# Performance work log

Hardware: AMD Instinct MI355X
Metric: run time of the kernel (lower is better)

Reference implementation:

```python
import math
import jax, jax.numpy as jnp
import numpy as np

B, S, HIDDEN = 1, 8192, 2048
NUM_HEADS = 16
HEAD_DIM = HIDDEN // NUM_HEADS
NUM_FW = 4
FW_DIM = HIDDEN // NUM_FW
D_H = FW_DIM  # inter_multi = 1.0
WINDOW = 256
CHUNK = 2048
ROPE_THETA = 500000.0
BASE_LR_INV = float(np.log(np.expm1(0.001)))  # inv_softplus(1e-3)


def rms_norm(x, w, eps=1e-6):
    return x * jax.lax.rsqrt(jnp.mean(x * x, axis=-1, keepdims=True) + eps) * w


def apply_rope(q, k, theta):
    D = q.shape[-1]
    inv = 1.0 / (theta ** (jnp.arange(0, D, 2, dtype=jnp.float32) / D))
    t = jnp.arange(q.shape[1], dtype=jnp.float32)
    f = t[:, None] * inv[None, :]  # [S, D/2]
    cos = jnp.cos(f)[None, :, None, :]
    sin = jnp.sin(f)[None, :, None, :]
    def ap(x):
        x1, x2 = jnp.split(x, 2, axis=-1)
        return jnp.concatenate([x1 * cos - x2 * sin, x2 * cos + x1 * sin], axis=-1)
    return ap(q), ap(k)


def sliding_window_attn(q, k, v, window):
    # q,k,v: [B,S,H,D]; causal window of `window` tokens incl. self (flash (window-1, 0))
    B_, S_, H_, D_ = q.shape
    W = window
    nc = S_ // W
    def blk(x):
        return x.transpose(0, 2, 1, 3).reshape(B_, H_, nc, W, D_)
    qb, kb, vb = blk(q), blk(k), blk(v)
    pad = jnp.zeros((B_, H_, 1, W, D_), q.dtype)
    k2 = jnp.concatenate([jnp.concatenate([pad, kb[:, :, :-1]], 2), kb], 3)  # [B,H,nc,2W,D]
    v2 = jnp.concatenate([jnp.concatenate([pad, vb[:, :, :-1]], 2), vb], 3)
    r = jnp.arange(W)[:, None]
    j = jnp.arange(2 * W)[None, :]
    base = (j >= r + 1) & (j <= W + r)  # causal + within-window
    keypos = (jnp.arange(nc)[:, None, None] - 1) * W + j[None]
    mask = base[None] & (keypos >= 0)  # [nc,W,2W]
    scores = jnp.einsum('bhnqd,bhnkd->bhnqk', qb, k2) * (1.0 / math.sqrt(D_))
    scores = jnp.where(mask[None, None], scores, -jnp.inf)
    p = jax.nn.softmax(scores, axis=-1)
    o = jnp.einsum('bhnqk,bhnkd->bhnqd', p, v2)
    return o.reshape(B_, H_, S_, D_).transpose(0, 2, 1, 3)


def ttt_swiglu(fq, fk, fv, l0, l1, l2, w0, w1, w2, chunk):
    # fq/fk/fv: [BN,S,d]; l*: [BN,S,1]; w0,w2: [BN,dh,d]; w1: [BN,d,dh]
    BN, S_, d = fq.shape
    nc = S_ // chunk
    def ch(x):
        return x.reshape(BN, nc, chunk, x.shape[-1]).transpose(1, 0, 2, 3)
    xs = (ch(fq), ch(fk), ch(fv), ch(l0), ch(l1), ch(l2))
    def step(carry, x):
        w0c, w1c, w2c = carry
        qi, ki, vi, lr0, lr1, lr2 = x
        # apply current fast weights to chunk queries (SwiGLU MLP)
        o = jnp.einsum('bch,boh->bco',
                       jax.nn.silu(jnp.einsum('bcd,bhd->bch', qi, w0c)) * jnp.einsum('bcd,bhd->bch', qi, w2c),
                       w1c)
        # manual gradient of dot-product TTT loss L = -sum(v * f(k))
        g = jnp.einsum('bcd,bhd->bch', ki, w0c)
        hm = jnp.einsum('bcd,bhd->bch', ki, w2c)
        sg = jax.nn.sigmoid(g)
        silu_g = g * sg
        hid = silu_g * hm
        dhid = jnp.einsum('bco,boh->bch', vi, w1c)
        dhm = dhid * silu_g
        dg = dhid * hm
        dgp = dg * (sg * (1.0 + g * (1.0 - sg)))  # silu backprop
        w0n = w0c + jnp.einsum('bch,bcd->bhd', dgp * lr0, ki)
        w2n = w2c + jnp.einsum('bch,bcd->bhd', dhm * lr2, ki)
        w1n = w1c + jnp.einsum('bco,bch->boh', vi * lr1, hid)
        return (w0n, w1n, w2n), o
    _, outs = jax.lax.scan(step, (w0, w1, w2), xs)
    return outs.transpose(1, 0, 2, 3).reshape(BN, S_, d)


def setup_inputs():
    key = jax.random.key(0)
    ks = jax.random.split(key, 8)
    h = HIDDEN
    return {
        'hidden_states': jax.random.normal(ks[0], (B, S, h), jnp.float32),
        'qkv_w': jax.random.normal(ks[1], (3 * h, h), jnp.float32) * 0.02,
        'q_norm_w': jnp.ones((h,), jnp.float32),
        'k_norm_w': jnp.ones((h,), jnp.float32),
        'qk_scale': jnp.ones((h, 2), jnp.float32),
        'qk_offset': jnp.zeros((h, 2), jnp.float32),
        'lr_w': jax.random.normal(ks[2], (3 * NUM_FW, h), jnp.float32) * 0.02,
        'lr_b': jnp.zeros((3 * NUM_FW,), jnp.float32),
        'w0': jax.random.normal(ks[3], (NUM_FW, D_H, FW_DIM), jnp.float32) / math.sqrt(FW_DIM),
        'w1': jax.random.normal(ks[4], (NUM_FW, FW_DIM, D_H), jnp.float32) / math.sqrt(D_H),
        'w2': jax.random.normal(ks[5], (NUM_FW, D_H, FW_DIM), jnp.float32) / math.sqrt(FW_DIM),
        'ttt_norm_w': jnp.ones((FW_DIM,), jnp.float32),
        'o_proj_w': jax.random.normal(ks[6], (h, h), jnp.float32) * 0.02,
    }


def reference(hidden_states, qkv_w, q_norm_w, k_norm_w, qk_scale, qk_offset,
              lr_w, lr_b, w0, w1, w2, ttt_norm_w, o_proj_w):
    qkv = hidden_states @ qkv_w.T
    q, k, v = jnp.split(qkv, 3, axis=-1)
    q = rms_norm(q, q_norm_w)
    k = rms_norm(k, k_norm_w)
    # rescale q/k for the fast-weight path
    fq = q * qk_scale[:, 0] + qk_offset[:, 0]
    fk = k * qk_scale[:, 1] + qk_offset[:, 1]
    fv = v
    # windowed RoPE attention path
    qh = q.reshape(B, S, NUM_HEADS, HEAD_DIM)
    kh = k.reshape(B, S, NUM_HEADS, HEAD_DIM)
    vh = v.reshape(B, S, NUM_HEADS, HEAD_DIM)
    qh, kh = apply_rope(qh, kh, ROPE_THETA)
    attn_o = sliding_window_attn(qh, kh, vh, WINDOW).reshape(B, S, HIDDEN)
    # fast-weight (TTT) path: silu + per-head l2-norm on q/k
    fq = jax.nn.silu(fq).reshape(B, S, NUM_FW, FW_DIM)
    fk = jax.nn.silu(fk).reshape(B, S, NUM_FW, FW_DIM)
    fv = jax.nn.silu(fv).reshape(B, S, NUM_FW, FW_DIM)
    fq = fq / jnp.maximum(jnp.linalg.norm(fq, axis=-1, keepdims=True), 1e-12)
    fk = fk / jnp.maximum(jnp.linalg.norm(fk, axis=-1, keepdims=True), 1e-12)
    def flat(x):
        return x.transpose(0, 2, 1, 3).reshape(B * NUM_FW, S, FW_DIM)
    # per-token learning rates (mamba parameterization)
    lr = jax.nn.softplus(hidden_states @ lr_w.T + lr_b + BASE_LR_INV)  # [B,S,3*NH]
    l0, l1, l2 = jnp.split(lr, 3, axis=-1)
    def flat_lr(x):
        return x.transpose(0, 2, 1).reshape(B * NUM_FW, S, 1)
    def bcast(w):
        return jnp.broadcast_to(w[None], (B,) + w.shape).reshape(B * NUM_FW, w.shape[1], w.shape[2])
    o_fast = ttt_swiglu(flat(fq), flat(fk), flat(fv),
                        flat_lr(l0), flat_lr(l1), flat_lr(l2),
                        bcast(w0), bcast(w1), bcast(w2), CHUNK)
    o_fast = rms_norm(o_fast.reshape(B, NUM_FW, S, FW_DIM), ttt_norm_w)
    o_fast = o_fast.transpose(0, 2, 1, 3).reshape(B, S, HIDDEN)
    return (attn_o + o_fast) @ o_proj_w.T
```

## Files before the change

### kernel.cpp

```cpp
#include <hip/hip_runtime.h>
#include <hip/hip_bf16.h>

typedef __hip_bfloat16 bf16;
typedef __bf16 bft;
typedef bft bf16x8 __attribute__((ext_vector_type(8)));
typedef bft bf16x4 __attribute__((ext_vector_type(4)));
typedef float f32x4 __attribute__((ext_vector_type(4)));

#define S_LEN 8192
#define HID   2048
#define QKV3  6144
#define NH    16
#define HD    128
#define NFW   4
#define FD    512
#define CHUNK_LEN 2048
#define NCHUNK 4
#define BASE_LR_INV (-6.9072552f)
#define QKP 136
#define VSP 72
#define PSP 76

__device__ __forceinline__ float bf2f(bf16 x){ return __bfloat162float(x); }
__device__ __forceinline__ bf16  f2bf(float x){ return __float2bfloat16(x); }
__device__ __forceinline__ float sigm(float x){ return 1.f/(1.f+__expf(-x)); }
__device__ __forceinline__ float siluf(float x){ return x/(1.f+__expf(-x)); }
__device__ __forceinline__ float wave_sum(float v){
  #pragma unroll
  for(int off=32; off; off>>=1) v += __shfl_xor(v, off, 64);
  return v;
}

template<int N>
__device__ __forceinline__ void waitcnt_vm(){
  static_assert(N==0||N==2||N==4||N==8, "unsupported vmcnt");
  if constexpr (N==0)      asm volatile("s_waitcnt vmcnt(0)" ::: "memory");
  else if constexpr (N==2) asm volatile("s_waitcnt vmcnt(2)" ::: "memory");
  else if constexpr (N==4) asm volatile("s_waitcnt vmcnt(4)" ::: "memory");
  else                     asm volatile("s_waitcnt vmcnt(8)" ::: "memory");
}

__device__ __forceinline__ void bar(){
  __builtin_amdgcn_s_barrier();
  asm volatile("" ::: "memory");
}

template<int ROWS>
__device__ __forceinline__ void stage(const bft* __restrict__ src, long ld,
                                      bft* dst, int tid)
{
  const int lane = tid & 63, wv = tid >> 6;
  #pragma unroll
  for (int i = 0; i < ROWS/64; ++i) {
    const int r0 = wv*16 + i*64;
    const int row = r0 + (lane >> 2);
    const int g = (lane & 3) ^ ((row >> 1) & 3);
    const bft* gp = src + (size_t)row*ld + g*8;
    bft* lp = dst + (size_t)r0*32;
    __builtin_amdgcn_global_load_lds(
        (const __attribute__((address_space(1))) void*)gp,
        (__attribute__((address_space(3))) void*)lp, 16, 0, 0);
  }
}

template<int BM,int BN,int EPI>
__global__ __launch_bounds__(256) void mgemm_k(
    const bft* __restrict__ A, const bft* __restrict__ B, void* __restrict__ Cv,
    bft* __restrict__ Cd, bft* __restrict__ Ct, int K,
    long lda, long ldb, long ldc, long sA, long sB, long sC)
{
  constexpr int AM = BM/32, AN = BN/32;
  constexpr int LPT = BM/64 + BN/64;
  constexpr int NPH = (AM >= 4) ? 2 : 1;
  constexpr int MH  = AM / NPH;
  __shared__ __align__(16) bft As[4][BM*32];
  __shared__ __align__(16) bft Bs[4][BN*32];
  const int tid = threadIdx.x;
  const int z = blockIdx.z;
  A += (size_t)z * sA;
  B += (size_t)z * sB;
  const size_t m0 = (size_t)blockIdx.y * BM, n0 = (size_t)blockIdx.x * BN;
  const int wv = tid >> 6, lane = tid & 63;
  const int wm = (wv & 1) * (BM/2), wn = (wv >> 1) * (BN/2);
  const int fr = lane & 15;
  const int fsw = ((lane >> 4) ^ ((fr >> 1) & 3)) * 8;

  f32x4 acc[AM][AN];
  #pragma unroll
  for (int i=0;i<AM;i++)
    #pragma unroll
    for (int j=0;j<AN;j++) acc[i][j] = (f32x4){0.f,0.f,0.f,0.f};

  const bft* Ab = A + m0*lda;
  const bft* Bb = B + n0*ldb;
  const int NS = K >> 5;

  stage<BM>(Ab,      lda, As[0], tid);
  stage<BN>(Bb,      ldb, Bs[0], tid);
  stage<BM>(Ab + 32, lda, As[1], tid);
  stage<BN>(Bb + 32, ldb, Bs[1], tid);
  waitcnt_vm<LPT>();
  bar();

  for (int s = 0; s < NS; ++s) {
    const bft* Ap = As[s & 3];
    const bft* Bp = Bs[s & 3];
    const int kt = (s + 2) * 32;
    const bool st = (s + 2 < NS);

    bf16x8 bvv[AN], afv[MH];
    #pragma unroll
    for (int ni=0; ni<AN; ni++)
      bvv[ni] = *(const bf16x8*)(Bp + (size_t)(wn + ni*16 + fr)*32 + fsw);
    #pragma unroll
    for (int i=0; i<MH; i++)
      afv[i] = *(const bf16x8*)(Ap + (size_t)(wm + i*16 + fr)*32 + fsw);
    if (st) stage<BM>(Ab + kt, lda, As[(s+2)&3], tid);
    if constexpr (NPH == 1) {
      if (st) { stage<BN>(Bb + kt, ldb, Bs[(s+2)&3], tid); waitcnt_vm<LPT>(); }
      else waitcnt_vm<0>();
    }
    bar();
    __builtin_amdgcn_s_setprio(1);
    #pragma unroll
    for (int i=0; i<MH; i++)
      #pragma unroll
      for (int ni=0; ni<AN; ni++)
        acc[i][ni] = __builtin_amdgcn_mfma_f32_16x16x32_bf16(afv[i], bvv[ni], acc[i][ni], 0, 0, 0);
    __builtin_amdgcn_s_setprio(0);

    if constexpr (NPH == 2) {
      bar();
      #pragma unroll
      for (int i=0; i<MH; i++)
        afv[i] = *(const bf16x8*)(Ap + (size_t)(wm + (MH+i)*16 + fr)*32 + fsw);
      if (st) { stage<BN>(Bb + kt, ldb, Bs[(s+2)&3], tid); waitcnt_vm<LPT>(); }
      else waitcnt_vm<0>();
      bar();
      __builtin_amdgcn_s_setprio(1);
      #pragma unroll
      for (int i=0; i<MH; i++)
        #pragma unroll
        for (int ni=0; ni<AN; ni++)
          acc[MH+i][ni] = __builtin_amdgcn_mfma_f32_16x16x32_bf16(afv[i], bvv[ni], acc[MH+i][ni], 0, 0, 0);
      __builtin_amdgcn_s_setprio(0);
      bar();
    }
  }

  const int er = (lane >> 4) * 4;
  const int ec = lane & 15;
  #pragma unroll
  for (int mi=0; mi<AM; mi++){
    #pragma unroll
    for (int ni=0; ni<AN; ni++){
      #pragma unroll
      for (int r=0; r<4; r++){
        size_t row = m0 + wm + mi*16 + er + r;
        size_t col = n0 + wn + ni*16 + ec;
        size_t idx = (size_t)z*sC + row*ldc + col;
        float v = acc[mi][ni][r];
        if constexpr (EPI == 0){
          ((bft*)Cv)[idx] = (bft)v;
        } else if constexpr (EPI == 1){
          ((float*)Cv)[idx] = v;
        } else {
          float nv = ((float*)Cv)[idx] + v;
          ((float*)Cv)[idx] = nv;
          Cd[idx] = (bft)nv;
          if (Ct) Ct[(size_t)z*FD*FD + col*FD + row] = (bft)nv;
        }
      }
    }
  }
}

template<int BM,int BN,int EPI>
static inline void mgemm(hipStream_t st, const bft* A, const bft* B, void* C,
    bft* Cd, bft* Ct, int M, int N, int K, long lda, long ldb, long ldc,
    int batch, long sA, long sB, long sC)
{
  dim3 g(N/BN, M/BM, batch);
  mgemm_k<BM,BN,EPI><<<g, 256, 0, st>>>(A, B, C, Cd, Ct, K, lda, ldb, ldc, sA, sB, sC);
}

__device__ __forceinline__ void stage8(const bft* __restrict__ src, long ld,
                                       bft* dst, int tid)
{
  const int lane = tid & 63, wv = tid >> 6;
  #pragma unroll
  for (int i = 0; i < 2; ++i) {
    const int r0 = wv*16 + i*128;
    const int row = r0 + (lane >> 2);
    const int g = (lane & 3) ^ ((row >> 1) & 3);
    const bft* gp = src + (size_t)row*ld + g*8;
    bft* lp = dst + (size_t)r0*32;
    __builtin_amdgcn_global_load_lds(
        (const __attribute__((address_space(1))) void*)gp,
        (__attribute__((address_space(3))) void*)lp, 16, 0, 0);
  }
}

#define M8_ROW(mi, a) { \
    acc[mi][0]=__builtin_amdgcn_mfma_f32_16x16x32_bf16(a,bv[0],acc[mi][0],0,0,0); \
    acc[mi][1]=__builtin_amdgcn_mfma_f32_16x16x32_bf16(a,bv[1],acc[mi][1],0,0,0); \
    acc[mi][2]=__builtin_amdgcn_mfma_f32_16x16x32_bf16(a,bv[2],acc[mi][2],0,0,0); \
    acc[mi][3]=__builtin_amdgcn_mfma_f32_16x16x32_bf16(a,bv[3],acc[mi][3],0,0,0); }

template<int EPI>
__global__ __launch_bounds__(512, 2) void mgemm8_k(
    const bft* __restrict__ A, const bft* __restrict__ B, void* __restrict__ Cv,
    int K, long lda, long ldb, long ldc)
{
  __shared__ __align__(16) bft As[4][256*32];
  __shared__ __align__(16) bft Bs[4][256*32];
  const int tid = threadIdx.x;

  const int gx = (int)gridDim.x;
  const int nwg = (int)(gridDim.x * gridDim.y);
  int lin = (int)(blockIdx.y * gridDim.x + blockIdx.x);
  if ((nwg & 7) == 0) lin = (lin & 7) * (nwg >> 3) + (lin >> 3);
  const size_t m0 = (size_t)(lin / gx) * 256;
  const size_t n0 = (size_t)(lin % gx) * 256;

  const int wv = tid >> 6, lane = tid & 63;
  const int wm = (wv & 1) * 128, wn = (wv >> 1) * 64;
  const int fr = lane & 15;
  const int fsw = ((lane >> 4) ^ ((fr >> 1) & 3)) * 8;

  f32x4 acc[8][4];
  #pragma unroll
  for (int i=0;i<8;i++)
    #pragma unroll
    for (int j=0;j<4;j++) acc[i][j] = (f32x4){0.f,0.f,0.f,0.f};

  const bft* Ab = A + m0*lda;
  const bft* Bb = B + n0*ldb;
  const int NS = K >> 5;

  stage8(Ab,      lda, As[0], tid);
  stage8(Bb,      ldb, Bs[0], tid);
  stage8(Ab + 32, lda, As[1], tid);
  stage8(Bb + 32, ldb, Bs[1], tid);
  waitcnt_vm<4>();
  bar();

  for (int s = 0; s < NS; ++s) {
    const bft* Ap = As[s & 3];
    const bft* Bp = Bs[s & 3];
    const int kt = (s + 2) * 32;
    const bool st = (s + 2 < NS);
    bf16x8 bv[4], a0, a1, a2, a3;

    bv[0] = *(const bf16x8*)(Bp + (size_t)(wn +  0 + fr)*32 + fsw);
    bv[1] = *(const bf16x8*)(Bp + (size_t)(wn + 16 + fr)*32 + fsw);
    bv[2] = *(const bf16x8*)(Bp + (size_t)(wn + 32 + fr)*32 + fsw);
    bv[3] = *(const bf16x8*)(Bp + (size_t)(wn + 48 + fr)*32 + fsw);
    a0 = *(const bf16x8*)(Ap + (size_t)(wm +  0 + fr)*32 + fsw);
    a1 = *(const bf16x8*)(Ap + (size_t)(wm + 16 + fr)*32 + fsw);
    a2 = *(const bf16x8*)(Ap + (size_t)(wm + 32 + fr)*32 + fsw);
    a3 = *(const bf16x8*)(Ap + (size_t)(wm + 48 + fr)*32 + fsw);
    if (st) stage8(Ab + kt, lda, As[(s+2)&3], tid);
    bar();
    __builtin_amdgcn_s_setprio(1);
    M8_ROW(0, a0); M8_ROW(1, a1); M8_ROW(2, a2); M8_ROW(3, a3);
    __builtin_amdgcn_s_setprio(0);
    bar();

    a0 = *(const bf16x8*)(Ap + (size_t)(wm +  64 + fr)*32 + fsw);
    a1 = *(const bf16x8*)(Ap + (size_t)(wm +  80 + fr)*32 + fsw);
    a2 = *(const bf16x8*)(Ap + (size_t)(wm +  96 + fr)*32 + fsw);
    a3 = *(const bf16x8*)(Ap + (size_t)(wm + 112 + fr)*32 + fsw);
    if (st) { stage8(Bb + kt, ldb, Bs[(s+2)&3], tid); waitcnt_vm<4>(); }
    else waitcnt_vm<0>();
    bar();
    __builtin_amdgcn_s_setprio(1);
    M8_ROW(4, a0); M8_ROW(5, a1); M8_ROW(6, a2); M8_ROW(7, a3);
    __builtin_amdgcn_s_setprio(0);
    bar();
  }

  const int er = (lane >> 4) * 4;
  const int ec = lane & 15;
  #pragma unroll
  for (int mi=0; mi<8; mi++){
    #pragma unroll
    for (int ni=0; ni<4; ni++){
      #pragma unroll
      for (int r=0; r<4; r++){
        size_t row = m0 + wm + mi*16 + er + r;
        size_t col = n0 + wn + ni*16 + ec;
        size_t idx = row*ldc + col;
        float v = acc[mi][ni][r];
        if constexpr (EPI == 0) ((bft*)Cv)[idx] = (bft)v;
        else                    ((float*)Cv)[idx] = v;
      }
    }
  }
}

template<int EPI>
static inline void mgemm8(hipStream_t st, const bft* A, const bft* B, void* C,
                          int M, int N, int K, long lda, long ldb, long ldc)
{
  dim3 g(N/256, M/256, 1);
  mgemm8_k<EPI><<<g, 512, 0, st>>>(A, B, C, K, lda, ldb, ldc);
}

__global__ __launch_bounds__(256) void cvt_k(const float* __restrict__ s,
    bft* __restrict__ d)
{
  size_t i = ((size_t)blockIdx.x*256 + threadIdx.x) * 8;
  const float4 v0 = *(const float4*)(s + i);
  const float4 v1 = *(const float4*)(s + i + 4);
  bf16x8 b;
  b[0]=(bft)v0.x; b[1]=(bft)v0.y; b[2]=(bft)v0.z; b[3]=(bft)v0.w;
  b[4]=(bft)v1.x; b[5]=(bft)v1.y; b[6]=(bft)v1.z; b[7]=(bft)v1.w;
  *(bf16x8*)(d + i) = b;
}

__global__ __launch_bounds__(256) void tr_k(const bft* __restrict__ in,
    bft* __restrict__ out, long ldin, long sIn, long sOut)
{
  __shared__ __align__(16) bft t[64][72];
  const int c0 = blockIdx.x*64, r0 = blockIdx.y*64;
  in  += (size_t)blockIdx.z * sIn;
  out += (size_t)blockIdx.z * sOut;
  const int tid = threadIdx.x;
  #pragma unroll
  for (int i=0;i<2;i++){
    int e = tid + i*256;
    int r = e >> 3, c8 = (e & 7) * 8;
    *(bf16x8*)&t[r][c8] = *(const bf16x8*)(in + (size_t)(r0+r)*ldin + c0 + c8);
  }
  __syncthreads();
  #pragma unroll
  for (int i=0;i<2;i++){
    int e = tid + i*256;
    int c = e >> 3, r8 = (e & 7) * 8;
    bf16x8 v;
    #pragma unroll
    for (int j=0;j<8;j++) v[j] = t[r8+j][c];
    *(bf16x8*)(out + (size_t)(c0+c)*CHUNK_LEN + r0 + r8) = v;
  }
}

__global__ __launch_bounds__(256) void tcw1_k(const float* __restrict__ w1,
    bft* __restrict__ w1tb)
{
  size_t idx = (size_t)blockIdx.x*256 + threadIdx.x;
  int z = (int)(idx >> 18);
  int h = (int)((idx >> 9) & 511);
  int o = (int)(idx & 511);
  w1tb[idx] = (bft)w1[(size_t)z*FD*FD + (size_t)o*FD + h];
}

__global__ __launch_bounds__(256) void vt_k(const bf16* __restrict__ qkv,
    bft* __restrict__ vT)
{
  __shared__ __align__(16) bft t[64*QKP];
  const int s0 = blockIdx.x * 64;
  const int h  = blockIdx.y;
  const int tid = threadIdx.x;
  #pragma unroll
  for (int i=0;i<4;i++){
    int e = tid + i*256;
    int rr = e >> 4, doff = (e & 15) * 8;
    *(bf16x8*)(t + rr*QKP + doff) =
        *(const bf16x8*)((const bft*)qkv + (size_t)(s0+rr)*QKV3 + 2*HID + h*HD + doff);
  }
  __syncthreads();
  #pragma unroll
  for (int it=0; it<4; it++){
    int d = (tid >> 3) + it*32;
    int so8 = (tid & 7) * 8;
    bf16x8 v;
    #pragma unroll
    for (int j=0;j<8;j++) v[j] = t[(so8+j)*QKP + d];
    *(bf16x8*)(vT + ((size_t)(h*HD + d))*S_LEN + s0 + so8) = v;
  }
}

__global__ void rope_k(float* __restrict__ rc, float* __restrict__ rs){
  int pos = blockIdx.x, d = threadIdx.x;
  float inv = 1.f / powf(500000.0f, (float)d * (1.0f/64.0f));
  float ang = (float)pos * inv;
  rc[pos*64+d] = cosf(ang);
  rs[pos*64+d] = sinf(ang);
}

__global__ __launch_bounds__(256) void lr_k(const float* __restrict__ hidden,
    const float* __restrict__ lr_w, const float* __restrict__ lr_b,
    float* __restrict__ lro)
{
  __shared__ float hrow[HID];
  __shared__ float red[4][12];
  int s = blockIdx.x, tid = threadIdx.x;
  for(int i=0;i<HID/256;i++) hrow[tid+256*i] = hidden[(size_t)s*HID + tid + 256*i];
  __syncthreads();
  float part[12];
  #pragma unroll
  for(int o=0;o<12;o++) part[o]=0.f;
  for(int i=0;i<HID/256;i++){
    int j = tid + 256*i;
    float h = hrow[j];
    #pragma unroll
    for(int o=0;o<12;o++) part[o] += h * lr_w[o*HID + j];
  }
  int lane = tid & 63, w = tid >> 6;
  #pragma unroll
  for(int o=0;o<12;o++){
    float v = wave_sum(part[o]);
    if(lane==0) red[w][o] = v;
  }
  __syncthreads();
  if(tid < 12){
    float v = red[0][tid]+red[1][tid]+red[2][tid]+red[3][tid] + lr_b[tid] + BASE_LR_INV;
    float sp = (v > 20.f) ? v : log1pf(expf(v));
    lro[s*12 + tid] = sp;
  }
}

__global__ __launch_bounds__(256) void e2a_k(
    bf16* __restrict__ qkv,
    const float* __restrict__ qnw, const float* __restrict__ knw)
{
  __shared__ float red[8];
  int s = blockIdx.x, tid = threadIdx.x;
  int lane = tid & 63, w = tid >> 6;
  float qv[8], kv[8];
  float sq = 0.f, sk = 0.f;
  size_t base = (size_t)s*QKV3;
  #pragma unroll
  for(int i=0;i<8;i++){
    int j = tid*8 + i;
    qv[i] = bf2f(qkv[base + j]);
    kv[i] = bf2f(qkv[base + HID + j]);
    sq += qv[i]*qv[i]; sk += kv[i]*kv[i];
  }
  sq = wave_sum(sq); sk = wave_sum(sk);
  if(lane==0){ red[w] = sq; red[4+w] = sk; }
  __syncthreads();
  float rq = rsqrtf((red[0]+red[1]+red[2]+red[3])*(1.f/HID) + 1e-6f);
  float rk = rsqrtf((red[4]+red[5]+red[6]+red[7])*(1.f/HID) + 1e-6f);
  #pragma unroll
  for(int i=0;i<8;i++){
    int j = tid*8 + i;
    qkv[base + j]       = f2bf(qv[i]*rq*qnw[j]);
    qkv[base + HID + j] = f2bf(kv[i]*rk*knw[j]);
  }
}

__global__ __launch_bounds__(256) void e2b_k(
    bf16* __restrict__ qkv,
    const float* __restrict__ qks, const float* __restrict__ qko)
{
  int s = blockIdx.x, tid = threadIdx.x;
  size_t base = (size_t)s*QKV3;
  float a[8], b[8], vv[8];
  float ga = 0.f, gb2 = 0.f;
  #pragma unroll
  for(int i=0;i<8;i++){
    int j = tid*8 + i;
    float qn = bf2f(qkv[base + j]);
    float kn = bf2f(qkv[base + HID + j]);
    float v  = bf2f(qkv[base + 2*HID + j]);
    a[i] = siluf(qn*qks[2*j]   + qko[2*j]);
    b[i] = siluf(kn*qks[2*j+1] + qko[2*j+1]);
    vv[i] = siluf(v);
    ga += a[i]*a[i]; gb2 += b[i]*b[i];
  }
  ga = wave_sum(ga); gb2 = wave_sum(gb2);
  float iq = 1.f / fmaxf(sqrtf(ga), 1e-12f);
  float ik = 1.f / fmaxf(sqrtf(gb2), 1e-12f);
  #pragma unroll
  for(int i=0;i<8;i++){
    int j = tid*8 + i;
    qkv[base + j]         = f2bf(a[i]*iq);
    qkv[base + HID + j]   = f2bf(b[i]*ik);
    qkv[base + 2*HID + j] = f2bf(vv[i]);
  }
}

__global__ __launch_bounds__(256) void attn_k(
    const bf16* __restrict__ qkv, const bft* __restrict__ vT,
    const float* __restrict__ rc, const float* __restrict__ rs,
    float* __restrict__ attn)
{
  __shared__ __align__(16) bft Qs[64*QKP];
  __shared__ __align__(16) bft Ks[64*QKP];
  __shared__ __align__(16) bft Vs[128*VSP];
  __shared__ __align__(16) bft Ps[64*PSP];
  const int head = blockIdx.x >> 7;
  const int Q0 = (blockIdx.x & 127) * 64;
  const int tid = threadIdx.x;
  const int hb = head * HD;
  const int lane = tid & 63;
  const int wm = (tid >> 6) * 16;
  const int fr = lane & 15, fko = (lane >> 4) * 8;
  const int rbase = (lane >> 4) * 4;

  #pragma unroll
  for(int i=0;i<16;i++){
    int e = tid + i*256;
    int rr = e >> 6, d = e & 63;
    int qpos = Q0 + rr;
    size_t b = (size_t)qpos*QKV3 + hb;
    float x1 = bf2f(qkv[b + d]);
    float x2 = bf2f(qkv[b + d + 64]);
    float c = rc[qpos*64 + d], sn = rs[qpos*64 + d];
    Qs[rr*QKP + d]      = (bft)(x1*c - x2*sn);
    Qs[rr*QKP + d + 64] = (bft)(x2*c + x1*sn);
  }
  __syncthreads();
  bf16x8 qf[4];
  #pragma unroll
  for (int kk=0;kk<4;kk++)
    qf[kk] = *(const bf16x8*)(Qs + (wm+fr)*QKP + kk*32 + fko);

  f32x4 Ot[8];
  #pragma unroll
  for (int i=0;i<8;i++) Ot[i] = (f32x4){0.f,0.f,0.f,0.f};
  float m4[4], l4[4];
  #pragma unroll
  for (int r=0;r<4;r++){ m4[r] = -INFINITY; l4[r] = 0.f; }

  for (int kt=0; kt<5; kt++){
    const int kb = Q0 - 256 + kt*64;
    if (kb < 0) continue;
    __syncthreads();
    #pragma unroll
    for(int i=0;i<16;i++){
      int e = tid + i*256;
      int rr = e >> 6, d = e & 63;
      int kpos = kb + rr;
      size_t b = (size_t)kpos*QKV3 + HID + hb;
      float x1 = bf2f(qkv[b + d]);
      float x2 = bf2f(qkv[b + d + 64]);
      float c = rc[kpos*64 + d], sn = rs[kpos*64 + d];
      Ks[rr*QKP + d]      = (bft)(x1*c - x2*sn);
      Ks[rr*QKP + d + 64] = (bft)(x2*c + x1*sn);
    }
    {
      int d = tid >> 1, koff = (tid & 1) * 32;
      const bft* vrow = vT + ((size_t)(hb + d))*S_LEN + kb + koff;
      bft* lrow = Vs + d*VSP + koff;
      #pragma unroll
      for (int j8=0;j8<4;j8++)
        *(bf16x8*)(lrow + j8*8) = *(const bf16x8*)(vrow + j8*8);
    }
    __syncthreads();

    f32x4 st[4];
    #pragma unroll
    for (int nt=0;nt<4;nt++){
      f32x4 acc = (f32x4){0.f,0.f,0.f,0.f};
      #pragma unroll
      for (int kk=0;kk<4;kk++){
        bf16x8 kf = *(const bf16x8*)(Ks + (nt*16+fr)*QKP + kk*32 + fko);
        acc = __builtin_amdgcn_mfma_f32_16x16x32_bf16(qf[kk], kf, acc, 0, 0, 0);
      }
      st[nt] = acc;
    }

    float pv[4][4];
    #pragma unroll
    for (int r=0;r<4;r++){
      int qpos = Q0 + wm + rbase + r;
      float sm[4];
      float mx = -INFINITY;
      #pragma unroll
      for (int nt=0;nt<4;nt++){
        int kpos = kb + nt*16 + fr;
        bool valid = (kpos > qpos - 256) && (kpos <= qpos);
        float s = valid ? st[nt][r] * 0.088388347648318447f : -INFINITY;
        sm[nt] = s;
        mx = fmaxf(mx, s);
      }
      mx = fmaxf(mx, __shfl_xor(mx, 1, 64));
      mx = fmaxf(mx, __shfl_xor(mx, 2, 64));
      mx = fmaxf(mx, __shfl_xor(mx, 4, 64));
      mx = fmaxf(mx, __shfl_xor(mx, 8, 64));
      float mnew = fmaxf(m4[r], mx);
      float alpha = (mnew == -INFINITY) ? 1.f : __expf(m4[r] - mnew);
      float ps = 0.f;
      #pragma unroll
      for (int nt=0;nt<4;nt++){
        float p = (sm[nt] == -INFINITY) ? 0.f : __expf(sm[nt] - mnew);
        pv[nt][r] = p;
        ps += p;
      }
      ps += __shfl_xor(ps, 1, 64);
      ps += __shfl_xor(ps, 2, 64);
      ps += __shfl_xor(ps, 4, 64);
      ps += __shfl_xor(ps, 8, 64);
      l4[r] = l4[r]*alpha + ps;
      m4[r] = mnew;
      #pragma unroll
      for (int ct=0;ct<8;ct++) Ot[ct][r] *= alpha;
    }

    #pragma unroll
    for (int r=0;r<4;r++){
      int row = wm + rbase + r;
      #pragma unroll
      for (int nt=0;nt<4;nt++)
        Ps[row*PSP + nt*16 + fr] = (bft)pv[nt][r];
    }
    bf16x8 af[2];
    #pragma unroll
    for (int kk=0;kk<2;kk++){
      const bft* pp = Ps + (wm+fr)*PSP + kk*32 + fko;
      bf16x4 lo = *(const bf16x4*)pp;
      bf16x4 hi = *(const bf16x4*)(pp+4);
      bf16x8 a;
      #pragma unroll
      for (int j=0;j<4;j++){ a[j]=lo[j]; a[j+4]=hi[j]; }
      af[kk]=a;
    }
    #pragma unroll
    for (int ct=0;ct<8;ct++)
      #pragma unroll
      for (int kk=0;kk<2;kk++){
        bf16x8 bv = *(const bf16x8*)(Vs + (ct*16+fr)*VSP + kk*32 + fko);
        Ot[ct] = __builtin_amdgcn_mfma_f32_16x16x32_bf16(af[kk], bv, Ot[ct], 0, 0, 0);
      }
  }

  #pragma unroll
  for (int r=0;r<4;r++){
    float invl = 1.f / l4[r];
    int qpos = Q0 + wm + rbase + r;
    size_t ob = (size_t)qpos*HID + hb;
    #pragma unroll
    for (int ct=0;ct<8;ct++)
      attn[ob + ct*16 + fr] = Ot[ct][r] * invl;
  }
}

__global__ __launch_bounds__(256) void e3_k(
    const bf16* __restrict__ g, const bf16* __restrict__ hm,
    bf16* __restrict__ qg, const bf16* __restrict__ qm,
    bf16* __restrict__ hid)
{
  size_t idx = (size_t)blockIdx.x*256 + threadIdx.x;
  float opre = siluf(bf2f(qg[idx])) * bf2f(qm[idx]);
  hid[idx] = f2bf(siluf(bf2f(g[idx])) * bf2f(hm[idx]));
  qg[idx]  = f2bf(opre);
}

__global__ __launch_bounds__(256) void e4_k(
    bf16* __restrict__ g, bf16* __restrict__ hm, bf16* __restrict__ dhid,
    const bf16* __restrict__ qkv, const float* __restrict__ lrb, int cbase)
{
  size_t idx = (size_t)blockIdx.x*256 + threadIdx.x;
  int h  = (int)(idx >> 20);
  int ci = (int)((idx >> 9) & 2047);
  int d  = (int)(idx & 511);
  int s  = cbase + ci;
  float l0  = lrb[s*12 + h];
  float l1  = lrb[s*12 + 4 + h];
  float l2v = lrb[s*12 + 8 + h];
  float gg = bf2f(g[idx]), hv = bf2f(hm[idx]), dh = bf2f(dhid[idx]);
  float sg = sigm(gg);
  float silu_g = gg * sg;
  float dhm = dh * silu_g;
  float dg  = dh * hv;
  float dgp = dg * (sg * (1.f + gg * (1.f - sg)));
  float fvv = bf2f(qkv[(size_t)s*QKV3 + 2*HID + h*FD + d]);
  g[idx]    = f2bf(dgp * l0);
  hm[idx]   = f2bf(dhm * l2v);
  dhid[idx] = f2bf(fvv * l1);
}

__global__ __launch_bounds__(256) void e5_k(const float* __restrict__ attn,
    const bf16* __restrict__ ofc, const float* __restrict__ tnw,
    bf16* __restrict__ qkv, int cbase)
{
  int ci = blockIdx.x, tid = threadIdx.x;
  int s = cbase + ci;
  int lane = tid & 63, w = tid >> 6;
  float o[8]; float ss = 0.f;
  size_t ob = ((size_t)w*CHUNK_LEN + ci)*FD + (size_t)lane*8;
  #pragma unroll
  for(int i=0;i<8;i++){ o[i] = bf2f(ofc[ob+i]); ss += o[i]*o[i]; }
  ss = wave_sum(ss);
  float inv = rsqrtf(ss*(1.f/FD) + 1e-6f);
  size_t xb = (size_t)s*QKV3 + w*FD + (size_t)lane*8;
  size_t ab = (size_t)s*HID  + w*FD + (size_t)lane*8;
  #pragma unroll
  for(int i=0;i<8;i++){
    int d = lane*8 + i;
    qkv[xb+i] = f2bf(attn[ab+i] + o[i]*inv*tnw[d]);
  }
}

extern "C" void kernel_launch(void* const* d_in, const int* in_sizes, int n_in,
                              void* d_out, int out_size, void* d_ws, size_t ws_size,
                              hipStream_t stream)
{
  (void)in_sizes; (void)n_in; (void)out_size;
  const float* hidden   = (const float*)d_in[0];
  const float* qkv_w    = (const float*)d_in[1];
  const float* q_norm_w = (const float*)d_in[2];
  const float* k_norm_w = (const float*)d_in[3];
  const float* qk_scale = (const float*)d_in[4];
  const float* qk_off   = (const float*)d_in[5];
  const float* lr_w     = (const float*)d_in[6];
  const float* lr_b     = (const float*)d_in[7];
  const float* w0_in    = (const float*)d_in[8];
  const float* w1_in    = (const float*)d_in[9];
  const float* w2_in    = (const float*)d_in[10];
  const float* ttt_nw   = (const float*)d_in[11];
  const float* o_proj   = (const float*)d_in[12];
  float* out = (float*)d_out;

  char* p = (char*)d_ws;
  auto alloc = [&](size_t n){ char* r = p; p += (n + 255) & ~(size_t)255; return (void*)r; };

  bf16*  qkv   = (bf16*) alloc((size_t)S_LEN*QKV3*sizeof(bf16));
  float* lrb   = (float*)alloc((size_t)S_LEN*12*sizeof(float));
  float* rc    = (float*)alloc((size_t)S_LEN*64*sizeof(float));
  float* rs    = (float*)alloc((size_t)S_LEN*64*sizeof(float));
  float* w0s   = (float*)alloc((size_t)NFW*FD*FD*sizeof(float));
  float* w1s   = (float*)alloc((size_t)NFW*FD*FD*sizeof(float));
  float* w2s   = (float*)alloc((size_t)NFW*FD*FD*sizeof(float));
  bft*   w1tb  = (bft*)  alloc((size_t)NFW*FD*FD*sizeof(bft));
  bft*   w0b   = (bft*)  alloc((size_t)NFW*FD*FD*sizeof(bft));
  bft*   w1b   = (bft*)  alloc((size_t)NFW*FD*FD*sizeof(bft));
  bft*   w2b   = (bft*)  alloc((size_t)NFW*FD*FD*sizeof(bft));
  bf16*  gb    = (bf16*) alloc((size_t)NFW*CHUNK_LEN*FD*sizeof(bf16));
  bf16*  hmb   = (bf16*) alloc((size_t)NFW*CHUNK_LEN*FD*sizeof(bf16));
  bf16*  qgb   = (bf16*) alloc((size_t)NFW*CHUNK_LEN*FD*sizeof(bf16));
  bf16*  qmb   = (bf16*) alloc((size_t)NFW*CHUNK_LEN*FD*sizeof(bf16));
  bf16*  hidb  = (bf16*) alloc((size_t)NFW*CHUNK_LEN*FD*sizeof(bf16));
  bf16*  ofc   = (bf16*) alloc((size_t)NFW*CHUNK_LEN*FD*sizeof(bf16));
  bft*   fkT   = (bft*)  alloc((size_t)NFW*FD*CHUNK_LEN*sizeof(bft));
  bft*   hidT  = (bft*)  alloc((size_t)NFW*FD*CHUNK_LEN*sizeof(bft));
  bft*   a2T   = (bft*)  alloc((size_t)NFW*FD*CHUNK_LEN*sizeof(bft));
  bft*   a1T   = (bft*)  alloc((size_t)NFW*FD*CHUNK_LEN*sizeof(bft));

  if ((size_t)(p - (char*)d_ws) > ws_size) return;

  bft* hidden_bf = (bft*)gb;
  bft* qkvw_bf   = (bft*)fkT;
  bft* vT        = (bft*)fkT;
  bft* opw_bf    = (bft*)hidb;

  float* attn = out;

  hipMemcpyAsync(w0s, w0_in, (size_t)NFW*FD*FD*sizeof(float), hipMemcpyDeviceToDevice, stream);
  hipMemcpyAsync(w1s, w1_in, (size_t)NFW*FD*FD*sizeof(float), hipMemcpyDeviceToDevice, stream);
  hipMemcpyAsync(w2s, w2_in, (size_t)NFW*FD*FD*sizeof(float), hipMemcpyDeviceToDevice, stream);

  rope_k<<<S_LEN, 64, 0, stream>>>(rc, rs);
  lr_k<<<S_LEN, 256, 0, stream>>>(hidden, lr_w, lr_b, lrb);
  tcw1_k<<<NFW*FD*FD/256, 256, 0, stream>>>(w1_in, w1tb);
  cvt_k<<<(NFW*FD*FD)/2048, 256, 0, stream>>>(w0_in, w0b);
  cvt_k<<<(NFW*FD*FD)/2048, 256, 0, stream>>>(w1_in, w1b);
  cvt_k<<<(NFW*FD*FD)/2048, 256, 0, stream>>>(w2_in, w2b);
  cvt_k<<<(S_LEN*HID)/2048, 256, 0, stream>>>(hidden, hidden_bf);
  cvt_k<<<(QKV3*HID)/2048, 256, 0, stream>>>(qkv_w, qkvw_bf);

  mgemm8<0>(stream, hidden_bf, qkvw_bf, (void*)qkv, S_LEN, QKV3, HID, HID, HID, QKV3);

  e2a_k<<<S_LEN, 256, 0, stream>>>(qkv, q_norm_w, k_norm_w);
  vt_k<<<dim3(S_LEN/64, NH), 256, 0, stream>>>(qkv, vT);
  attn_k<<<NH*128, 256, 0, stream>>>(qkv, vT, rc, rs, attn);
  e2b_k<<<S_LEN, 256, 0, stream>>>(qkv, qk_scale, qk_off);

  const long sW  = (long)FD*FD;
  const long sCh = (long)CHUNK_LEN*FD;
  const long sT  = (long)FD*CHUNK_LEN;
  const int  NEL = NFW*CHUNK_LEN*FD/256;
  const dim3 tg(FD/64, CHUNK_LEN/64, NFW);

  for(int c=0; c<NCHUNK; c++){
    const bft* fqc = (const bft*)qkv + (size_t)c*CHUNK_LEN*QKV3;
    const bft* fkc = fqc + HID;
    const bft* fvc = fqc + 2*HID;
    mgemm<128,128,0>(stream, fkc, w0b, gb,  nullptr, nullptr, CHUNK_LEN, FD, FD, QKV3, FD, FD, NFW, FD, sW, sCh);
    mgemm<128,128,0>(stream, fkc, w2b, hmb, nullptr, nullptr, CHUNK_LEN, FD, FD, QKV3, FD, FD, NFW, FD, sW, sCh);
    mgemm<128,128,0>(stream, fqc, w0b, qgb, nullptr, nullptr, CHUNK_LEN, FD, FD, QKV3, FD, FD, NFW, FD, sW, sCh);
    mgemm<128,128,0>(stream, fqc, w2b, qmb, nullptr, nullptr, CHUNK_LEN, FD, FD, QKV3, FD, FD, NFW, FD, sW, sCh);
    e3_k<<<NEL, 256, 0, stream>>>(gb, hmb, qgb, qmb, hidb);
    mgemm<128,128,0>(stream, (const bft*)qgb, w1b, ofc, nullptr, nullptr, CHUNK_LEN, FD, FD, FD, FD, FD, NFW, sCh, sW, sCh);
    mgemm<128,128,0>(stream, fvc, (const bft*)w1tb, qmb, nullptr, nullptr, CHUNK_LEN, FD, FD, QKV3, FD, FD, NFW, FD, sW, sCh);
    e4_k<<<NEL, 256, 0, stream>>>(gb, hmb, qmb, qkv, lrb, c*CHUNK_LEN);
    tr_k<<<tg, 256, 0, stream>>>(fkc,              fkT,        QKV3, FD,  sT);
    tr_k<<<tg, 256, 0, stream>>>((const bft*)hidb, hidT,       FD,   sCh, sT);
    tr_k<<<tg, 256, 0, stream>>>((const bft*)gb,   (bft*)qgb,  FD,   sCh, sT);
    tr_k<<<tg, 256, 0, stream>>>((const bft*)hmb,  a2T,        FD,   sCh, sT);
    tr_k<<<tg, 256, 0, stream>>>((const bft*)qmb,  a1T,        FD,   sCh, sT);
    mgemm<64,64,2>(stream, (const bft*)qgb, fkT,  w0s, w0b, nullptr, FD, FD, CHUNK_LEN, CHUNK_LEN, CHUNK_LEN, FD, NFW, sT, sT, sW);
    mgemm<64,64,2>(stream, a2T,             fkT,  w2s, w2b, nullptr, FD, FD, CHUNK_LEN, CHUNK_LEN, CHUNK_LEN, FD, NFW, sT, sT, sW);
    mgemm<64,64,2>(stream, a1T,             hidT, w1s, w1b, w1tb,    FD, FD, CHUNK_LEN, CHUNK_LEN, CHUNK_LEN, FD, NFW, sT, sT, sW);
    e5_k<<<CHUNK_LEN, 256, 0, stream>>>(attn, ofc, ttt_nw, qkv, c*CHUNK_LEN);
  }

  cvt_k<<<(HID*HID)/2048, 256, 0, stream>>>(o_proj, opw_bf);
  mgemm8<1>(stream, (const bft*)qkv, opw_bf, out, S_LEN, HID, HID, QKV3, HID, HID);
}
```

Baseline: 1.548 ms.

## Concatenate w0/w2 fast weights so each chunk does two wide GEMMs instead of four

Packs the bf16 copies of w0 and w2 into one [1024,512] matrix per head, so the forward projections of fk and fq through both weights run as two N=1024 GEMMs instead of four N=512 launches. The elementwise kernels are rewritten to read and write the interleaved [chunk,1024] buffers, and one transpose scratch buffer is reused between the three weight-update GEMMs. This cuts kernel launches and reuses the A-operand tile across both weights. In exchange it adds per-head conversion launches at setup and serializes the transposes with the update GEMMs through the shared scratch buffer.

```diff
diff --git a/kernel.cpp b/kernel.cpp
--- a/kernel.cpp
+++ b/kernel.cpp
@@ -67,7 +67,7 @@
 __global__ __launch_bounds__(256) void mgemm_k(
     const bft* __restrict__ A, const bft* __restrict__ B, void* __restrict__ Cv,
     bft* __restrict__ Cd, bft* __restrict__ Ct, int K,
-    long lda, long ldb, long ldc, long sA, long sB, long sC)
+    long lda, long ldb, long ldc, long sA, long sB, long sC, long sCd)
 {
   constexpr int AM = BM/32, AN = BN/32;
   constexpr int LPT = BM/64 + BN/64;
@@ -167,7 +167,7 @@
         } else {
           float nv = ((float*)Cv)[idx] + v;
           ((float*)Cv)[idx] = nv;
-          Cd[idx] = (bft)nv;
+          Cd[(size_t)z*sCd + row*ldc + col] = (bft)nv;
           if (Ct) Ct[(size_t)z*FD*FD + col*FD + row] = (bft)nv;
         }
       }
@@ -178,10 +178,10 @@
 template<int BM,int BN,int EPI>
 static inline void mgemm(hipStream_t st, const bft* A, const bft* B, void* C,
     bft* Cd, bft* Ct, int M, int N, int K, long lda, long ldb, long ldc,
-    int batch, long sA, long sB, long sC)
+    int batch, long sA, long sB, long sC, long sCd)
 {
   dim3 g(N/BN, M/BM, batch);
-  mgemm_k<BM,BN,EPI><<<g, 256, 0, st>>>(A, B, C, Cd, Ct, K, lda, ldb, ldc, sA, sB, sC);
+  mgemm_k<BM,BN,EPI><<<g, 256, 0, st>>>(A, B, C, Cd, Ct, K, lda, ldb, ldc, sA, sB, sC, sCd);
 }
 
 __device__ __forceinline__ void stage8(const bft* __restrict__ src, long ld,
@@ -638,39 +638,42 @@
   }
 }
 
-__global__ __launch_bounds__(256) void e3_k(
-    const bf16* __restrict__ g, const bf16* __restrict__ hm,
-    bf16* __restrict__ qg, const bf16* __restrict__ qm,
-    bf16* __restrict__ hid)
+__global__ __launch_bounds__(256) void e3f_k(
+    bft* __restrict__ gh, bft* __restrict__ qgm, bft* __restrict__ hid)
 {
   size_t idx = (size_t)blockIdx.x*256 + threadIdx.x;
-  float opre = siluf(bf2f(qg[idx])) * bf2f(qm[idx]);
-  hid[idx] = f2bf(siluf(bf2f(g[idx])) * bf2f(hm[idx]));
-  qg[idx]  = f2bf(opre);
-}
-
-__global__ __launch_bounds__(256) void e4_k(
-    bf16* __restrict__ g, bf16* __restrict__ hm, bf16* __restrict__ dhid,
+  int z  = (int)(idx >> 20);
+  int ci = (int)((idx >> 9) & 2047);
+  int d  = (int)(idx & 511);
+  size_t b = ((size_t)z*CHUNK_LEN + ci)*1024 + d;
+  float opre = siluf((float)qgm[b]) * (float)qgm[b + 512];
+  hid[idx] = (bft)(siluf((float)gh[b]) * (float)gh[b + 512]);
+  qgm[b]   = (bft)opre;
+}
+
+__global__ __launch_bounds__(256) void e4f_k(
+    bft* __restrict__ gh, bft* __restrict__ qgm,
     const bf16* __restrict__ qkv, const float* __restrict__ lrb, int cbase)
 {
   size_t idx = (size_t)blockIdx.x*256 + threadIdx.x;
-  int h  = (int)(idx >> 20);
+  int z  = (int)(idx >> 20);
   int ci = (int)((idx >> 9) & 2047);
   int d  = (int)(idx & 511);
   int s  = cbase + ci;
-  float l0  = lrb[s*12 + h];
-  float l1  = lrb[s*12 + 4 + h];
-  float l2v = lrb[s*12 + 8 + h];
-  float gg = bf2f(g[idx]), hv = bf2f(hm[idx]), dh = bf2f(dhid[idx]);
+  float l0  = lrb[s*12 + z];
+  float l1  = lrb[s*12 + 4 + z];
+  float l2v = lrb[s*12 + 8 + z];
+  size_t b = ((size_t)z*CHUNK_LEN + ci)*1024 + d;
+  float gg = (float)gh[b], hv = (float)gh[b + 512], dh = (float)qgm[b + 512];
   float sg = sigm(gg);
   float silu_g = gg * sg;
   float dhm = dh * silu_g;
   float dg  = dh * hv;
   float dgp = dg * (sg * (1.f + gg * (1.f - sg)));
-  float fvv = bf2f(qkv[(size_t)s*QKV3 + 2*HID + h*FD + d]);
-  g[idx]    = f2bf(dgp * l0);
-  hm[idx]   = f2bf(dhm * l2v);
-  dhid[idx] = f2bf(fvv * l1);
+  float fvv = bf2f(qkv[(size_t)s*QKV3 + 2*HID + z*FD + d]);
+  gh[b]        = (bft)(dgp * l0);
+  gh[b + 512]  = (bft)(dhm * l2v);
+  qgm[b + 512] = (bft)(fvv * l1);
 }
 
 __global__ __launch_bounds__(256) void e5_k(const float* __restrict__ attn,
@@ -726,9 +729,8 @@
   float* w1s   = (float*)alloc((size_t)NFW*FD*FD*sizeof(float));
   float* w2s   = (float*)alloc((size_t)NFW*FD*FD*sizeof(float));
   bft*   w1tb  = (bft*)  alloc((size_t)NFW*FD*FD*sizeof(bft));
-  bft*   w0b   = (bft*)  alloc((size_t)NFW*FD*FD*sizeof(bft));
+  bft*   w02b  = (bft*)  alloc((size_t)NFW*1024*FD*sizeof(bft));
   bft*   w1b   = (bft*)  alloc((size_t)NFW*FD*FD*sizeof(bft));
-  bft*   w2b   = (bft*)  alloc((size_t)NFW*FD*FD*sizeof(bft));
   bf16*  gb    = (bf16*) alloc((size_t)NFW*CHUNK_LEN*FD*sizeof(bf16));
   bf16*  hmb   = (bf16*) alloc((size_t)NFW*CHUNK_LEN*FD*sizeof(bf16));
   bf16*  qgb   = (bf16*) alloc((size_t)NFW*CHUNK_LEN*FD*sizeof(bf16));
@@ -738,10 +740,11 @@
   bft*   fkT   = (bft*)  alloc((size_t)NFW*FD*CHUNK_LEN*sizeof(bft));
   bft*   hidT  = (bft*)  alloc((size_t)NFW*FD*CHUNK_LEN*sizeof(bft));
   bft*   a2T   = (bft*)  alloc((size_t)NFW*FD*CHUNK_LEN*sizeof(bft));
-  bft*   a1T   = (bft*)  alloc((size_t)NFW*FD*CHUNK_LEN*sizeof(bft));
 
   if ((size_t)(p - (char*)d_ws) > ws_size) return;
 
+  bft* ghb = (bft*)gb;
+  bft* qgm = (bft*)qgb;
   bft* hidden_bf = (bft*)gb;
   bft* qkvw_bf   = (bft*)fkT;
   bft* vT        = (bft*)fkT;
@@ -749,6 +752,12 @@
 
   float* attn = out;
 
+  const long sW  = (long)FD*FD;
+  const long sW2 = (long)1024*FD;
+  const long sCh = (long)CHUNK_LEN*FD;
+  const long sGH = (long)CHUNK_LEN*1024;
+  const long sT  = (long)FD*CHUNK_LEN;
+
   hipMemcpyAsync(w0s, w0_in, (size_t)NFW*FD*FD*sizeof(float), hipMemcpyDeviceToDevice, stream);
   hipMemcpyAsync(w1s, w1_in, (size_t)NFW*FD*FD*sizeof(float), hipMemcpyDeviceToDevice, stream);
   hipMemcpyAsync(w2s, w2_in, (size_t)NFW*FD*FD*sizeof(float), hipMemcpyDeviceToDevice, stream);
@@ -756,9 +765,11 @@
   rope_k<<<S_LEN, 64, 0, stream>>>(rc, rs);
   lr_k<<<S_LEN, 256, 0, stream>>>(hidden, lr_w, lr_b, lrb);
   tcw1_k<<<NFW*FD*FD/256, 256, 0, stream>>>(w1_in, w1tb);
-  cvt_k<<<(NFW*FD*FD)/2048, 256, 0, stream>>>(w0_in, w0b);
   cvt_k<<<(NFW*FD*FD)/2048, 256, 0, stream>>>(w1_in, w1b);
-  cvt_k<<<(NFW*FD*FD)/2048, 256, 0, stream>>>(w2_in, w2b);
+  for (int z = 0; z < NFW; ++z) {
+    cvt_k<<<(FD*FD)/2048, 256, 0, stream>>>(w0_in + (size_t)z*sW, w02b + (size_t)z*sW2);
+    cvt_k<<<(FD*FD)/2048, 256, 0, stream>>>(w2_in + (size_t)z*sW, w02b + (size_t)z*sW2 + (size_t)512*FD);
+  }
   cvt_k<<<(S_LEN*HID)/2048, 256, 0, stream>>>(hidden, hidden_bf);
   cvt_k<<<(QKV3*HID)/2048, 256, 0, stream>>>(qkv_w, qkvw_bf);
 
@@ -769,9 +780,6 @@
   attn_k<<<NH*128, 256, 0, stream>>>(qkv, vT, rc, rs, attn);
   e2b_k<<<S_LEN, 256, 0, stream>>>(qkv, qk_scale, qk_off);
 
-  const long sW  = (long)FD*FD;
-  const long sCh = (long)CHUNK_LEN*FD;
-  const long sT  = (long)FD*CHUNK_LEN;
   const int  NEL = NFW*CHUNK_LEN*FD/256;
   const dim3 tg(FD/64, CHUNK_LEN/64, NFW);
 
@@ -779,22 +787,27 @@
     const bft* fqc = (const bft*)qkv + (size_t)c*CHUNK_LEN*QKV3;
     const bft* fkc = fqc + HID;
     const bft* fvc = fqc + 2*HID;
-    mgemm<128,128,0>(stream, fkc, w0b, gb,  nullptr, nullptr, CHUNK_LEN, FD, FD, QKV3, FD, FD, NFW, FD, sW, sCh);
-    mgemm<128,128,0>(stream, fkc, w2b, hmb, nullptr, nullptr, CHUNK_LEN, FD, FD, QKV3, FD, FD, NFW, FD, sW, sCh);
-    mgemm<128,128,0>(stream, fqc, w0b, qgb, nullptr, nullptr, CHUNK_LEN, FD, FD, QKV3, FD, FD, NFW, FD, sW, sCh);
-    mgemm<128,128,0>(stream, fqc, w2b, qmb, nullptr, nullptr, CHUNK_LEN, FD, FD, QKV3, FD, FD, NFW, FD, sW, sCh);
-    e3_k<<<NEL, 256, 0, stream>>>(gb, hmb, qgb, qmb, hidb);
-    mgemm<128,128,0>(stream, (const bft*)qgb, w1b, ofc, nullptr, nullptr, CHUNK_LEN, FD, FD, FD, FD, FD, NFW, sCh, sW, sCh);
-    mgemm<128,128,0>(stream, fvc, (const bft*)w1tb, qmb, nullptr, nullptr, CHUNK_LEN, FD, FD, QKV3, FD, FD, NFW, FD, sW, sCh);
-    e4_k<<<NEL, 256, 0, stream>>>(gb, hmb, qmb, qkv, lrb, c*CHUNK_LEN);
-    tr_k<<<tg, 256, 0, stream>>>(fkc,              fkT,        QKV3, FD,  sT);
-    tr_k<<<tg, 256, 0, stream>>>((const bft*)hidb, hidT,       FD,   sCh, sT);
-    tr_k<<<tg, 256, 0, stream>>>((const bft*)gb,   (bft*)qgb,  FD,   sCh, sT);
-    tr_k<<<tg, 256, 0, stream>>>((const bft*)hmb,  a2T,        FD,   sCh, sT);
-    tr_k<<<tg, 256, 0, stream>>>((const bft*)qmb,  a1T,        FD,   sCh, sT);
-    mgemm<64,64,2>(stream, (const bft*)qgb, fkT,  w0s, w0b, nullptr, FD, FD, CHUNK_LEN, CHUNK_LEN, CHUNK_LEN, FD, NFW, sT, sT, sW);
-    mgemm<64,64,2>(stream, a2T,             fkT,  w2s, w2b, nullptr, FD, FD, CHUNK_LEN, CHUNK_LEN, CHUNK_LEN, FD, NFW, sT, sT, sW);
-    mgemm<64,64,2>(stream, a1T,             hidT, w1s, w1b, w1tb,    FD, FD, CHUNK_LEN, CHUNK_LEN, CHUNK_LEN, FD, NFW, sT, sT, sW);
+    mgemm<128,128,0>(stream, fkc, w02b, ghb, nullptr, nullptr,
+        CHUNK_LEN, 1024, FD, QKV3, FD, 1024, NFW, FD, sW2, sGH, 0);
+    mgemm<128,128,0>(stream, fqc, w02b, qgm, nullptr, nullptr,
+        CHUNK_LEN, 1024, FD, QKV3, FD, 1024, NFW, FD, sW2, sGH, 0);
+    e3f_k<<<NEL, 256, 0, stream>>>(ghb, qgm, (bft*)hidb);
+    mgemm<128,128,0>(stream, (const bft*)qgm, w1b, ofc, nullptr, nullptr,
+        CHUNK_LEN, FD, FD, 1024, FD, FD, NFW, sGH, sW, sCh, 0);
+    mgemm<128,128,0>(stream, fvc, (const bft*)w1tb, qgm + 512, nullptr, nullptr,
+        CHUNK_LEN, FD, FD, QKV3, FD, 1024, NFW, FD, sW, sGH, 0);
+    e4f_k<<<NEL, 256, 0, stream>>>(ghb, qgm, qkv, lrb, c*CHUNK_LEN);
+    tr_k<<<tg, 256, 0, stream>>>(fkc,              fkT,  QKV3, FD,  sT);
+    tr_k<<<tg, 256, 0, stream>>>((const bft*)hidb, hidT, FD,   sCh, sT);
+    tr_k<<<tg, 256, 0, stream>>>(ghb,       a2T, 1024, sGH, sT);
+    mgemm<64,64,2>(stream, a2T, fkT,  w0s, w02b, nullptr,
+        FD, FD, CHUNK_LEN, CHUNK_LEN, CHUNK_LEN, FD, NFW, sT, sT, sW, sW2);
+    tr_k<<<tg, 256, 0, stream>>>(ghb + 512, a2T, 1024, sGH, sT);
+    mgemm<64,64,2>(stream, a2T, fkT,  w2s, w02b + (size_t)512*FD, nullptr,
+        FD, FD, CHUNK_LEN, CHUNK_LEN, CHUNK_LEN, FD, NFW, sT, sT, sW, sW2);
+    tr_k<<<tg, 256, 0, stream>>>(qgm + 512, a2T, 1024, sGH, sT);
+    mgemm<64,64,2>(stream, a2T, hidT, w1s, w1b, w1tb,
+        FD, FD, CHUNK_LEN, CHUNK_LEN, CHUNK_LEN, FD, NFW, sT, sT, sW, sW);
     e5_k<<<CHUNK_LEN, 256, 0, stream>>>(attn, ofc, ttt_nw, qkv, c*CHUNK_LEN);
   }
 
```

Measured after the change: 1.507 ms. -2.7%, faster.
